# Optimization experiments

Measured on AMD Instinct MI355X. Metric: run time of the kernel, lower is better.

## Reference

```python
import jax, jax.numpy as jnp
import numpy as np

B, C, N, V, W, D = 4, 64, 8, 32, 32, 256  # spa_dim = D


def _ln(x, g, b, eps=1e-5):
    m = jnp.mean(x, -1, keepdims=True)
    v = jnp.mean((x - m) ** 2, -1, keepdims=True)
    return (x - m) * jax.lax.rsqrt(v + eps) * g + b


def _tokens(x):
    # (b, c, n, v, w) -> (b*n, v*w, c)
    b, c, n, v, w = x.shape
    return x.transpose(0, 2, 3, 4, 1).reshape(b * n, v * w, c)


def setup_inputs() -> dict:
    key = jax.random.key(0)
    ks = jax.random.split(key, 8)
    fea_lf = jax.random.normal(ks[0], (B, C, N, V, W), jnp.float32)
    fea_hf = jax.random.normal(ks[1], (B, C, N, V, W), jnp.float32)
    W_in = jax.random.normal(ks[2], (C, D), jnp.float32) / np.sqrt(C)
    W_kv = jax.random.normal(ks[3], (C, 2 * D), jnp.float32) / np.sqrt(C)
    gamma = jnp.ones((D,), jnp.float32)
    beta = jnp.zeros((D,), jnp.float32)
    g2 = jnp.ones((D,), jnp.float32)
    b2 = jnp.zeros((D,), jnp.float32)
    W1 = jax.random.normal(ks[4], (D, 2 * D), jnp.float32) / np.sqrt(D)
    W2 = jax.random.normal(ks[5], (2 * D, D), jnp.float32) / np.sqrt(2 * D)
    W_out = jax.random.normal(ks[6], (D, C), jnp.float32) / np.sqrt(D)
    return {"fea_lf": fea_lf, "fea_hf": fea_hf, "W_in": W_in, "W_kv": W_kv,
            "gamma": gamma, "beta": beta, "g2": g2, "b2": b2,
            "W1": W1, "W2": W2, "W_out": W_out}


def reference(fea_lf, fea_hf, W_in, W_kv, gamma, beta, g2, b2, W1, W2, W_out):
    b, c, n, v, w = fea_lf.shape
    S = v * w
    tok_q = _tokens(fea_lf)   # (bn, S, c)
    tok_kv = _tokens(fea_hf)  # (bn, S, c)
    q = _ln(tok_q @ W_in, gamma, beta)              # (bn, S, D)
    kv = tok_kv @ W_kv
    k, vtok = jnp.split(kv, 2, axis=-1)
    k = _ln(k, gamma, beta)                          # shared LayerNorm (self.norm)
    # NOTE: original has no 1/sqrt(d) scaling on scores.
    score = jnp.einsum('bqd,bkd->bqk', q, k)         # (bn, S, S)
    mask = jnp.tril(jnp.ones((S, S), bool))
    score = jnp.where(mask, score, jnp.float32(-1e15))
    p = jax.nn.softmax(score, axis=-1)
    att = jnp.einsum('bqk,bkd->bqd', p, vtok)        # (bn, S, D)
    h = jax.nn.relu(_ln(att, g2, b2) @ W1) @ W2      # FFN (dropout=0)
    epi = h + vtok
    out = epi @ W_out                                # (bn, S, c)
    return out.reshape(b, n, v, w, c).transpose(0, 4, 1, 2, 3)
```

## Files before the change

kernel.cpp:

```cpp
#include <hip/hip_runtime.h>

typedef short bf16x8 __attribute__((ext_vector_type(8)));
typedef _Float16 f16x8 __attribute__((ext_vector_type(8)));
typedef float f32x4 __attribute__((ext_vector_type(4)));
typedef unsigned short u16;
typedef unsigned short u16x4 __attribute__((ext_vector_type(4)));

#define MFMA(a, b, c) __builtin_amdgcn_mfma_f32_16x16x32_bf16(a, b, c, 0, 0, 0)
#define MFMAH(a, b, c) __builtin_amdgcn_mfma_f32_16x16x32_f16(a, b, c, 0, 0, 0)

__device__ __forceinline__ u16 f2b(float f) {
    union { float f; unsigned u; } x{f};
    unsigned r = (x.u + 0x7FFFu + ((x.u >> 16) & 1u)) >> 16;
    return (u16)r;
}
__device__ __forceinline__ float b2f(u16 h) {
    union { unsigned u; float f; } x{((unsigned)h) << 16};
    return x.f;
}
__device__ __forceinline__ u16 f2h(float f) {
    _Float16 h = (_Float16)f;
    return *reinterpret_cast<u16*>(&h);
}
__device__ __forceinline__ float h2f(u16 h) {
    _Float16 v = *reinterpret_cast<_Float16*>(&h);
    return (float)v;
}
__device__ __forceinline__ float red16_sum(float v) {
#pragma unroll
    for (int m = 1; m < 16; m <<= 1) v += __shfl_xor(v, m, 64);
    return v;
}
__device__ __forceinline__ float red16_max(float v) {
#pragma unroll
    for (int m = 1; m < 16; m <<= 1) v = fmaxf(v, __shfl_xor(v, m, 64));
    return v;
}
__device__ __forceinline__ void gl_lds16(const void* g, void* l) {
    __builtin_amdgcn_global_load_lds(
        (const __attribute__((address_space(1))) unsigned int*)(g),
        (__attribute__((address_space(3))) unsigned int*)(l), 16, 0, 0);
}


__global__ __launch_bounds__(256) void wconv_kernel(
    const float* __restrict__ W1, const float* __restrict__ W2,
    const float* __restrict__ Wo, const float* __restrict__ Win,
    const float* __restrict__ Wkv, u16* __restrict__ w1T,
    u16* __restrict__ w2T, u16* __restrict__ woT, u16* __restrict__ wfrag) {
    int id = blockIdx.x * 256 + threadIdx.x;
    if (id < 131072) {
        int n = id >> 8, k = id & 255;
        w1T[id] = f2b(W1[k * 512 + n]);
    } else if (id < 262144) {
        int j = id - 131072;
        int n = j >> 9, k = j & 511;
        w2T[j] = f2b(W2[k * 256 + n]);
    } else if (id < 278528) {
        int j = id - 262144;
        int n = j >> 8, k = j & 255;
        woT[j] = f2b(Wo[k * 64 + n]);
    } else if (id < 284672) {
        int fid = id - 278528;
        int arr = fid >> 11;
        int e = fid & 2047;
        int ntck = e >> 6, ln = e & 63;
        int lr = ln & 15, lg2 = ln >> 4;
        int nt = ntck >> 1, ck = ntck & 1;
        int d = nt * 16 + lr;
#pragma unroll
        for (int j = 0; j < 8; j++) {
            int c = ck * 32 + lg2 * 8 + j;
            float x;
            if (arr == 0)      x = Win[c * 256 + d];
            else if (arr == 1) x = Wkv[c * 512 + d];
            else               x = Wkv[c * 512 + 256 + d];
            wfrag[arr * 16384 + e * 8 + j] = f2h(x);
        }
    }
}

#define PJ_A 0
#define PJ_WREG 16384
#define PJ_WORK 49152
__global__ __launch_bounds__(512, 1) void proj_kernel(
    const float* __restrict__ lf, const float* __restrict__ hf,
    const u16* __restrict__ wqg, const u16* __restrict__ wkg,
    const u16* __restrict__ wvg, const float* __restrict__ gamma,
    const float* __restrict__ beta, u16* __restrict__ qf_,
    u16* __restrict__ kf_, u16* __restrict__ vT) {
    extern __shared__ char sm[];
    const int tid = threadIdx.x;
    const int wave = tid >> 6, lane = tid & 63, lr = lane & 15, lg = lane >> 4;
    const int st = blockIdx.x, bn = blockIdx.y;
    const int b = bn >> 3, n = bn & 7;
    const int s0 = st * 128;
    const size_t baseF = (size_t)b * 524288 + (size_t)n * 1024 + s0;

    float gam[16], bet[16];
#pragma unroll
    for (int nt = 0; nt < 16; nt++) {
        gam[nt] = gamma[nt * 16 + lr];
        bet[nt] = beta[nt * 16 + lr];
    }

    auto stage32 = [&](const float* srcbase, int chalf) {
#pragma unroll
        for (int call = 0; call < 2; call++) {
            int unit = call * 8 + wave;
            int obase = unit << 10;
            int e = unit * 256 + lane * 4;
            int cl = e >> 7, si = e & 127;
            gl_lds16(srcbase + (size_t)(chalf * 32 + cl) * 8192 + si,
                     sm + PJ_WORK + obase);
        }
    };
    auto stageW = [&](const u16* wsrc) {
#pragma unroll
        for (int call = 0; call < 4; call++) {
            int obase = (call * 8 + wave) << 10;
            gl_lds16((const char*)wsrc + obase + lane * 16, sm + PJ_WREG + obase);
        }
    };
    auto buildA = [&](int slotbase) {
        int g = wave >> 1;
        int s = ((wave & 1) << 6) | lane;
        float x[8];
#pragma unroll
        for (int cc = 0; cc < 8; cc++)
            x[cc] = *(const float*)(sm + PJ_WORK + ((g * 8 + cc) << 9) + (s << 2));
        f16x8 ph;
#pragma unroll
        for (int cc = 0; cc < 8; cc++) ph[cc] = (_Float16)x[cc];
        int slp = (slotbase + g) ^ (s & 7);
        *(f16x8*)(sm + PJ_A + (s << 7) + (slp << 4)) = ph;
    };
    auto loadA = [&](f16x8* aF) {
        int tl = wave * 16 + lr;
#pragma unroll
        for (int ck = 0; ck < 2; ck++) {
            int off = (tl << 7) + ((((ck << 2) | lg) ^ (tl & 7)) << 4);
            aF[ck] = *(const f16x8*)(sm + PJ_A + off);
        }
    };
    auto pass1 = [&](const f16x8* aF, f32x4* acc) {
#pragma unroll
        for (int nt = 0; nt < 16; nt++) acc[nt] = (f32x4){0.f, 0.f, 0.f, 0.f};
#pragma unroll
        for (int nt = 0; nt < 16; nt++) {
#pragma unroll
            for (int ck = 0; ck < 2; ck++) {
                int wo = (((nt << 1) | ck) << 10) + (lane << 4);
                f16x8 bh = *(const f16x8*)(sm + PJ_WREG + wo);
                acc[nt] = MFMAH(aF[ck], bh, acc[nt]);
            }
        }
    };
    auto lnstats = [&](const f32x4* acc, float* mean, float* rs) {
#pragma unroll
        for (int r = 0; r < 4; r++) {
            float s1 = 0.f, s2 = 0.f;
#pragma unroll
            for (int nt = 0; nt < 16; nt++) {
                float xv = acc[nt][r];
                s1 += xv; s2 += xv * xv;
            }
            s1 = red16_sum(s1);
            s2 = red16_sum(s2);
            float mn = s1 * (1.f / 256.f);
            float var = s2 * (1.f / 256.f) - mn * mn;
            mean[r] = mn;
            rs[r] = rsqrtf(var + 1e-5f);
        }
    };
    auto emit = [&](const f32x4* acc, const float* mean, const float* rs,
                    u16* dst) {
        char* bw = sm + PJ_WORK + wave * 4096;
        const int gtok = bn * 1024 + s0 + wave * 16;
#pragma unroll
        for (int hh = 0; hh < 2; hh++) {
#pragma unroll
            for (int ntl = 0; ntl < 8; ntl++) {
                int nt = hh * 8 + ntl;
#pragma unroll
                for (int r = 0; r < 4; r++) {
                    float y = (acc[nt][r] - mean[r]) * rs[r] * gam[nt] + bet[nt];
                    int tl = lg * 4 + r;
                    int dl = ntl * 16 + lr;
                    int sl = dl >> 3;
                    *(u16*)(bw + tl * 256 + ((sl ^ ((tl >> 2) & 3)) << 4) +
                            (dl & 7) * 2) = f2h(y);
                }
            }
#pragma unroll
            for (int p = 0; p < 4; p++) {
                int row = lane >> 2, slq = (lane & 3) + p * 4;
                bf16x8 v8 = *(const bf16x8*)(bw + row * 256 +
                                             ((slq ^ ((row >> 2) & 3)) << 4));
                *(bf16x8*)(dst + (size_t)(gtok + row) * 256 + hh * 128 +
                           slq * 8) = v8;
            }
        }
    };

    f32x4 acc[16];
    float mean[4], rs[4];
    f16x8 aF[2];

    stage32(lf + baseF, 0);  __syncthreads();
    buildA(0);               __syncthreads();
    stage32(lf + baseF, 1);
    stageW(wqg);             __syncthreads();
    buildA(4);               __syncthreads();
    loadA(aF);
    pass1(aF, acc);
    lnstats(acc, mean, rs);  __syncthreads();
    stageW(wkg);
    emit(acc, mean, rs, qf_);
    __syncthreads();
    stage32(hf + baseF, 0);  __syncthreads();
    buildA(0);               __syncthreads();
    stage32(hf + baseF, 1);  __syncthreads();
    buildA(4);               __syncthreads();
    loadA(aF);
    pass1(aF, acc);
    lnstats(acc, mean, rs);  __syncthreads();
    stageW(wvg);
    emit(acc, mean, rs, kf_);
    __syncthreads();
    pass1(aF, acc);
#pragma unroll
    for (int nt = 0; nt < 16; nt++) {
        u16x4 pv;
#pragma unroll
        for (int r = 0; r < 4; r++) pv[r] = f2h(acc[nt][r]);
        *(u16x4*)(vT + ((size_t)(bn * 256) + nt * 16 + lr) * 1024 + s0 +
                  wave * 16 + lg * 4) = pv;
    }
}

__global__ __launch_bounds__(512) void attn_kernel(
    const u16* __restrict__ qf_, const u16* __restrict__ kf_,
    const u16* __restrict__ vT, const float* __restrict__ g2,
    const float* __restrict__ b2, u16* __restrict__ lnatt) {
    extern __shared__ char smem[];
    const int tid = threadIdx.x;
    const int wave = tid >> 6, lane = tid & 63, lr = lane & 15, lg = lane >> 4;
    const int grp = wave >> 2, w4 = wave & 3;
    const int b = blockIdx.x;
    const int bn = b & 31;
    const int strip = 15 - (b >> 5);
    const int qr0 = strip * 64 + w4 * 16;
    const int ni = strip + 1;
    const int ktbase = grp * ni;
    char* myK = smem + grp * 65536;
    char* myV = smem + grp * 65536 + 32768;
    u16* Pw = (u16*)(smem + 131072 + wave * 1280);

    f16x8 qf[8];
    {
        const size_t off = ((size_t)(bn * 1024 + qr0 + lr)) * 256 + lg * 8;
#pragma unroll
        for (int ck = 0; ck < 8; ck++)
            qf[ck] = *(const f16x8*)(qf_ + off + ck * 32);
    }
    f16x8 onesb;
    {
        _Float16 v1 = (lr == 0) ? (_Float16)1.0f : (_Float16)0.0f;
#pragma unroll
        for (int q = 0; q < 8; q++) onesb[q] = v1;
    }

    const int srl = lane >> 5, ss = lane & 31;
    const int vdl = lane >> 2, vg = lane & 3;
    auto stage = [&](int buf, int kt) {
        const int kv0 = kt << 5;
        char* baseK = myK + buf * 16384;
        char* baseV = myV + buf * 16384;
#pragma unroll
        for (int ii = 0; ii < 4; ii++) {
            int u = w4 * 4 + ii;
            int r = u * 2 + srl;
            size_t go = (((size_t)((bn << 10) + kv0 + r)) << 8) +
                        (unsigned)((ss ^ (r & 7)) << 3);
            gl_lds16(kf_ + go, baseK + u * 1024);
            int d = u * 16 + vdl;
            size_t gv = (((size_t)((bn << 8) + d)) << 10) + kv0 +
                        (unsigned)((vg ^ ((d >> 1) & 3)) << 3);
            gl_lds16(vT + gv, baseV + u * 1024);
        }
    };

    f32x4 o[16];
#pragma unroll
    for (int i = 0; i < 16; i++) o[i] = (f32x4){0.f, 0.f, 0.f, 0.f};
    f32x4 ol = (f32x4){0.f, 0.f, 0.f, 0.f};
    float m[4] = {-INFINITY, -INFINITY, -INFINITY, -INFINITY};

    stage(0, ktbase);
    for (int it = 0; it < ni; it++) {
        const int cur = it & 1;
        if (it + 1 < ni) {
            stage(cur ^ 1, ktbase + it + 1);
            asm volatile("s_waitcnt vmcnt(8)" ::: "memory");
        } else {
            asm volatile("s_waitcnt vmcnt(0)" ::: "memory");
        }
        __builtin_amdgcn_s_barrier();
        asm volatile("" ::: "memory");
        const int kt = ktbase + it;
        if ((kt << 5) <= qr0 + 15) {
            const char* kb = myK + cur * 16384;
            f32x4 sc0 = (f32x4){0.f, 0.f, 0.f, 0.f};
            f32x4 sc1 = (f32x4){0.f, 0.f, 0.f, 0.f};
            __builtin_amdgcn_s_setprio(1);
#pragma unroll
            for (int ck = 0; ck < 8; ck++) {
                int sw = ((ck * 4 + lg) ^ (lr & 7)) << 4;
                int a0 = lr * 512 + sw;
                f16x8 k0 = *(const f16x8*)(kb + a0);
                f16x8 k1 = *(const f16x8*)(kb + a0 + 8192);
                sc0 = MFMAH(qf[ck], k0, sc0);
                sc1 = MFMAH(qf[ck], k1, sc1);
            }
            __builtin_amdgcn_s_setprio(0);
            float scl[4];
            const int kvb = kt << 5;
#pragma unroll
            for (int r = 0; r < 4; r++) {
                int qi = qr0 + lg * 4 + r;
                float s0v = (kvb + lr > qi) ? -1e30f : sc0[r];
                float s1v = (kvb + 16 + lr > qi) ? -1e30f : sc1[r];
                float tm = red16_max(fmaxf(s0v, s1v));
                float mn = fmaxf(m[r], tm);
                scl[r] = __expf(m[r] - mn);
                m[r] = mn;
                int row = lg * 4 + r;
                Pw[row * 40 + lr] = f2h(__expf(s0v - mn));
                Pw[row * 40 + 16 + lr] = f2h(__expf(s1v - mn));
            }
#pragma unroll
            for (int f = 0; f < 16; f++) {
                f32x4 t = o[f];
                t[0] *= scl[0]; t[1] *= scl[1]; t[2] *= scl[2]; t[3] *= scl[3];
                o[f] = t;
            }
            ol[0] *= scl[0]; ol[1] *= scl[1]; ol[2] *= scl[2]; ol[3] *= scl[3];
            f16x8 pa = *(const f16x8*)((const char*)Pw + lr * 80 + lg * 16);
            const char* vb = myV + cur * 16384;
            __builtin_amdgcn_s_setprio(1);
#pragma unroll
            for (int db = 0; db < 16; db++) {
                int d = db * 16 + lr;
                f16x8 vf = *(const f16x8*)(vb + d * 64 +
                                           ((lg ^ ((lr >> 1) & 3)) << 4));
                o[db] = MFMAH(pa, vf, o[db]);
            }
            ol = MFMAH(pa, onesb, ol);
            __builtin_amdgcn_s_setprio(0);
        }
    }
    __syncthreads();
    float lsum[4];
#pragma unroll
    for (int r = 0; r < 4; r++) lsum[r] = __shfl(ol[r], lane & 48, 64);

    char* cb = smem + 65536;
    float* mlb = (float*)(smem + 131072);
    if (grp == 1) {
        char* po = cb + w4 * 16384;
#pragma unroll
        for (int f = 0; f < 16; f++)
            *(f32x4*)(po + (f * 16 + lr) * 64 + lg * 16) = o[f];
        if (lr == 0) {
#pragma unroll
            for (int r = 0; r < 4; r++) {
                int row = lg * 4 + r;
                mlb[(w4 * 16 + row) * 2] = m[r];
                mlb[(w4 * 16 + row) * 2 + 1] = lsum[r];
            }
        }
    }
    __syncthreads();
    if (grp == 0) {
        const char* po = cb + w4 * 16384;
        float e0[4], e1[4], linv[4];
#pragma unroll
        for (int r = 0; r < 4; r++) {
            int row = lg * 4 + r;
            float m1 = mlb[(w4 * 16 + row) * 2];
            float l1 = mlb[(w4 * 16 + row) * 2 + 1];
            float ms = fmaxf(m[r], m1);
            e0[r] = __expf(m[r] - ms);
            e1[r] = __expf(m1 - ms);
            linv[r] = 1.f / (lsum[r] * e0[r] + l1 * e1[r]);
        }
#pragma unroll
        for (int f = 0; f < 16; f++) {
            f32x4 o1 = *(const f32x4*)(po + (f * 16 + lr) * 64 + lg * 16);
#pragma unroll
            for (int r = 0; r < 4; r++)
                o[f][r] = (o[f][r] * e0[r] + o1[r] * e1[r]) * linv[r];
        }
        float gv[16], bv[16];
#pragma unroll
        for (int f = 0; f < 16; f++) {
            gv[f] = g2[f * 16 + lr];
            bv[f] = b2[f * 16 + lr];
        }
#pragma unroll
        for (int r = 0; r < 4; r++) {
            float s1 = 0.f, s2 = 0.f;
#pragma unroll
            for (int f = 0; f < 16; f++) {
                float x = o[f][r];
                s1 += x; s2 += x * x;
            }
            s1 = red16_sum(s1);
            s2 = red16_sum(s2);
            float mean = s1 * (1.f / 256.f);
            float var = s2 * (1.f / 256.f) - mean * mean;
            float rsv = rsqrtf(var + 1e-5f);
            size_t row = (size_t)(bn * 1024 + qr0 + lg * 4 + r) * 256;
#pragma unroll
            for (int f = 0; f < 16; f++)
                lnatt[row + f * 16 + lr] =
                    f2b((o[f][r] - mean) * rsv * gv[f] + bv[f]);
        }
    }
}

template <int K, int NB, int MODE>
__global__ __launch_bounds__(512) void gemmB_kernel(
    const u16* __restrict__ A, const u16* __restrict__ BT,
    u16* __restrict__ outb, const u16* __restrict__ vTr,
    float* __restrict__ outf, int ldOut) {
    extern __shared__ char bsm[];
    const int tid = threadIdx.x;
    const int wave = tid >> 6, lane = tid & 63, lr = lane & 15, lg = lane >> 4;
    constexpr int K2 = K * 2;
    constexpr int BN = NB * 16;
    constexpr int TILE = BN * K2;
    const int m0 = blockIdx.x * 128 + wave * 16;
    const int n0 = blockIdx.y * BN;
    {
        const char* bsrc = (const char*)(BT + (size_t)n0 * K);
        constexpr int ITER = TILE / (512 * 16);
#pragma unroll
        for (int it = 0; it < ITER; it++) {
            int o = (it * 512 + tid) * 16;
            int col = o / K2;
            int slot = (o % K2) >> 4;
            int src = col * K2 + ((slot ^ (col & 7)) << 4);
            gl_lds16(bsrc + src, bsm + o);
        }
    }
    __syncthreads();
    f32x4 acc[NB];
#pragma unroll
    for (int nb = 0; nb < NB; nb++) acc[nb] = (f32x4){0.f, 0.f, 0.f, 0.f};
    const u16* ap = A + (size_t)(m0 + lr) * K + lg * 8;
#pragma unroll
    for (int kc = 0; kc < K; kc += 32) {
        bf16x8 a = *(const bf16x8*)(ap + kc);
        int ks = (kc >> 3) + lg;
#pragma unroll
        for (int nb = 0; nb < NB; nb++) {
            int c = nb * 16 + lr;
            bf16x8 bv = *(const bf16x8*)(bsm + c * K2 + ((ks ^ (c & 7)) << 4));
            acc[nb] = MFMA(a, bv, acc[nb]);
        }
    }
    const int g = m0 + lg * 4;
    if (MODE == 0) {
#pragma unroll
        for (int nb = 0; nb < NB; nb++)
#pragma unroll
            for (int r = 0; r < 4; r++)
                outb[(size_t)(g + r) * ldOut + n0 + nb * 16 + lr] =
                    f2b(fmaxf(acc[nb][r], 0.f));
    } else if (MODE == 1) {
        int bn = g >> 10, s = g & 1023;
#pragma unroll
        for (int nb = 0; nb < NB; nb++) {
            int dd = n0 + nb * 16 + lr;
            u16x4 vv = *(const u16x4*)(vTr + ((size_t)bn * 256 + dd) * 1024 + s);
#pragma unroll
            for (int r = 0; r < 4; r++)
                outb[(size_t)(g + r) * 256 + dd] = f2b(acc[nb][r] + h2f(vv[r]));
        }
    } else {
        int bn = g >> 10, s = g & 1023;
        int bb = bn >> 3, nn = bn & 7;
#pragma unroll
        for (int nb = 0; nb < NB; nb++) {
            int cc = n0 + nb * 16 + lr;
            *(f32x4*)(outf + (size_t)bb * 524288 + (size_t)cc * 8192 +
                      (size_t)nn * 1024 + s) = acc[nb];
        }
    }
}

extern "C" void kernel_launch(void* const* d_in, const int* in_sizes, int n_in,
                              void* d_out, int out_size, void* d_ws, size_t ws_size,
                              hipStream_t stream) {
    const float* lf    = (const float*)d_in[0];
    const float* hf    = (const float*)d_in[1];
    const float* Win   = (const float*)d_in[2];
    const float* Wkv   = (const float*)d_in[3];
    const float* gamma = (const float*)d_in[4];
    const float* beta  = (const float*)d_in[5];
    const float* g2    = (const float*)d_in[6];
    const float* b2    = (const float*)d_in[7];
    const float* W1    = (const float*)d_in[8];
    const float* W2    = (const float*)d_in[9];
    const float* Wo    = (const float*)d_in[10];
    float* out = (float*)d_out;

    char* w = (char*)d_ws;
    const size_t MB16 = 16777216;
    u16* qf  = (u16*)(w);
    u16* kf  = (u16*)(w + MB16);
    u16* vT  = (u16*)(w + 2 * MB16);
    u16* hb  = (u16*)(w + 3 * MB16);
    u16* w1T = (u16*)(w + 3 * MB16 + 33554432);
    u16* w2T = w1T + 131072;
    u16* woT = w2T + 131072;
    u16* wfrag = woT + 16384;
    u16* wqg = wfrag;
    u16* wkg = wfrag + 16384;
    u16* wvg = wfrag + 32768;
    u16* lnatt = qf;
    u16* epib  = kf;

    wconv_kernel<<<dim3(1136), dim3(256), 0, stream>>>(W1, W2, Wo, Win, Wkv,
                                                       w1T, w2T, woT, wfrag);
    proj_kernel<<<dim3(8, 32), dim3(512), 81920, stream>>>(
        lf, hf, wqg, wkg, wvg, gamma, beta, qf, kf, vT);
    attn_kernel<<<dim3(512), dim3(512), 141312, stream>>>(qf, kf, vT, g2, b2,
                                                          lnatt);
    gemmB_kernel<256, 8, 0><<<dim3(256, 4), dim3(512), 65536, stream>>>(
        lnatt, w1T, hb, nullptr, nullptr, 512);
    gemmB_kernel<512, 8, 1><<<dim3(256, 2), dim3(512), 131072, stream>>>(
        hb, w2T, epib, vT, nullptr, 256);
    gemmB_kernel<256, 4, 2><<<dim3(256, 1), dim3(512), 32768, stream>>>(
        epib, woT, nullptr, nullptr, out, 64);
}
```

Baseline: 125.9 us.

## Restructure attention into 2-wave blocks with two row tiles per wave, no KV split

The attention kernel drops from 8 waves with a two-group KV split and double-buffered staging to 2 waves per block. Each wave now handles two 16-row query tiles, so every K/V fragment read from shared memory feeds twice as many MFMAs. The cross-group merge of partial softmax results is gone, and LDS use falls from about 138 KB to 37 KB, which allows more resident blocks per CU. In exchange, staging is no longer double-buffered, each block makes a serial pass over all KV tiles with a barrier per step, and register pressure roughly doubles for the accumulators.

```diff
diff --git a/kernel.cpp b/kernel.cpp
--- a/kernel.cpp
+++ b/kernel.cpp
@@ -239,30 +239,27 @@
     }
 }
 
-__global__ __launch_bounds__(512) void attn_kernel(
+__global__ __launch_bounds__(128) void attn_kernel(
     const u16* __restrict__ qf_, const u16* __restrict__ kf_,
     const u16* __restrict__ vT, const float* __restrict__ g2,
     const float* __restrict__ b2, u16* __restrict__ lnatt) {
-    extern __shared__ char smem[];
+    __shared__ char smem[37888];
     const int tid = threadIdx.x;
     const int wave = tid >> 6, lane = tid & 63, lr = lane & 15, lg = lane >> 4;
-    const int grp = wave >> 2, w4 = wave & 3;
     const int b = blockIdx.x;
     const int bn = b & 31;
     const int strip = 15 - (b >> 5);
-    const int qr0 = strip * 64 + w4 * 16;
-    const int ni = strip + 1;
-    const int ktbase = grp * ni;
-    char* myK = smem + grp * 65536;
-    char* myV = smem + grp * 65536 + 32768;
-    u16* Pw = (u16*)(smem + 131072 + wave * 1280);
-
-    f16x8 qf[8];
-    {
-        const size_t off = ((size_t)(bn * 1024 + qr0 + lr)) * 256 + lg * 8;
+    const int qr0 = strip * 64 + wave * 32;
+    const int ni = 2 * strip + 2;
+    u16* Pw = (u16*)(smem + 32768 + wave * 2560);
+
+    f16x8 qf[2][8];
+#pragma unroll
+    for (int rt = 0; rt < 2; rt++) {
+        const size_t off = ((size_t)(bn * 1024 + qr0 + rt * 16 + lr)) * 256 + lg * 8;
 #pragma unroll
         for (int ck = 0; ck < 8; ck++)
-            qf[ck] = *(const f16x8*)(qf_ + off + ck * 32);
+            qf[rt][ck] = *(const f16x8*)(qf_ + off + ck * 32);
     }
     f16x8 onesb;
     {
@@ -271,149 +268,126 @@
         for (int q = 0; q < 8; q++) onesb[q] = v1;
     }
 
-    const int srl = lane >> 5, ss = lane & 31;
-    const int vdl = lane >> 2, vg = lane & 3;
-    auto stage = [&](int buf, int kt) {
+    f32x4 o[2][16];
+#pragma unroll
+    for (int rt = 0; rt < 2; rt++)
+#pragma unroll
+        for (int i = 0; i < 16; i++) o[rt][i] = (f32x4){0.f, 0.f, 0.f, 0.f};
+    f32x4 ol[2] = {(f32x4){0.f, 0.f, 0.f, 0.f}, (f32x4){0.f, 0.f, 0.f, 0.f}};
+    float m[2][4];
+#pragma unroll
+    for (int rt = 0; rt < 2; rt++)
+#pragma unroll
+        for (int r = 0; r < 4; r++) m[rt][r] = -INFINITY;
+
+    for (int kt = 0; kt < ni; kt++) {
         const int kv0 = kt << 5;
-        char* baseK = myK + buf * 16384;
-        char* baseV = myV + buf * 16384;
-#pragma unroll
-        for (int ii = 0; ii < 4; ii++) {
-            int u = w4 * 4 + ii;
-            int r = u * 2 + srl;
+#pragma unroll
+        for (int u = 0; u < 8; u++) {
+            int ob = u * 2048 + tid * 16;
+            int r = ob >> 9;
+            int ss = tid & 31;
             size_t go = (((size_t)((bn << 10) + kv0 + r)) << 8) +
                         (unsigned)((ss ^ (r & 7)) << 3);
-            gl_lds16(kf_ + go, baseK + u * 1024);
-            int d = u * 16 + vdl;
+            gl_lds16(kf_ + go, smem + ob);
+            int d = u * 32 + (tid >> 2);
             size_t gv = (((size_t)((bn << 8) + d)) << 10) + kv0 +
-                        (unsigned)((vg ^ ((d >> 1) & 3)) << 3);
-            gl_lds16(vT + gv, baseV + u * 1024);
-        }
-    };
-
-    f32x4 o[16];
-#pragma unroll
-    for (int i = 0; i < 16; i++) o[i] = (f32x4){0.f, 0.f, 0.f, 0.f};
-    f32x4 ol = (f32x4){0.f, 0.f, 0.f, 0.f};
-    float m[4] = {-INFINITY, -INFINITY, -INFINITY, -INFINITY};
-
-    stage(0, ktbase);
-    for (int it = 0; it < ni; it++) {
-        const int cur = it & 1;
-        if (it + 1 < ni) {
-            stage(cur ^ 1, ktbase + it + 1);
-            asm volatile("s_waitcnt vmcnt(8)" ::: "memory");
-        } else {
-            asm volatile("s_waitcnt vmcnt(0)" ::: "memory");
-        }
-        __builtin_amdgcn_s_barrier();
-        asm volatile("" ::: "memory");
-        const int kt = ktbase + it;
-        if ((kt << 5) <= qr0 + 15) {
-            const char* kb = myK + cur * 16384;
-            f32x4 sc0 = (f32x4){0.f, 0.f, 0.f, 0.f};
-            f32x4 sc1 = (f32x4){0.f, 0.f, 0.f, 0.f};
+                        (unsigned)(((tid & 3) ^ ((d >> 1) & 3)) << 3);
+            gl_lds16(vT + gv, smem + 16384 + u * 2048 + tid * 16);
+        }
+        __syncthreads();
+        if (kv0 <= qr0 + 31) {
+            f32x4 sc00 = (f32x4){0.f, 0.f, 0.f, 0.f};
+            f32x4 sc01 = (f32x4){0.f, 0.f, 0.f, 0.f};
+            f32x4 sc10 = (f32x4){0.f, 0.f, 0.f, 0.f};
+            f32x4 sc11 = (f32x4){0.f, 0.f, 0.f, 0.f};
             __builtin_amdgcn_s_setprio(1);
 #pragma unroll
             for (int ck = 0; ck < 8; ck++) {
                 int sw = ((ck * 4 + lg) ^ (lr & 7)) << 4;
                 int a0 = lr * 512 + sw;
-                f16x8 k0 = *(const f16x8*)(kb + a0);
-                f16x8 k1 = *(const f16x8*)(kb + a0 + 8192);
-                sc0 = MFMAH(qf[ck], k0, sc0);
-                sc1 = MFMAH(qf[ck], k1, sc1);
+                f16x8 k0 = *(const f16x8*)(smem + a0);
+                f16x8 k1 = *(const f16x8*)(smem + a0 + 8192);
+                sc00 = MFMAH(qf[0][ck], k0, sc00);
+                sc01 = MFMAH(qf[0][ck], k1, sc01);
+                sc10 = MFMAH(qf[1][ck], k0, sc10);
+                sc11 = MFMAH(qf[1][ck], k1, sc11);
             }
             __builtin_amdgcn_s_setprio(0);
-            float scl[4];
-            const int kvb = kt << 5;
-#pragma unroll
-            for (int r = 0; r < 4; r++) {
-                int qi = qr0 + lg * 4 + r;
-                float s0v = (kvb + lr > qi) ? -1e30f : sc0[r];
-                float s1v = (kvb + 16 + lr > qi) ? -1e30f : sc1[r];
-                float tm = red16_max(fmaxf(s0v, s1v));
-                float mn = fmaxf(m[r], tm);
-                scl[r] = __expf(m[r] - mn);
-                m[r] = mn;
-                int row = lg * 4 + r;
-                Pw[row * 40 + lr] = f2h(__expf(s0v - mn));
-                Pw[row * 40 + 16 + lr] = f2h(__expf(s1v - mn));
-            }
-#pragma unroll
-            for (int f = 0; f < 16; f++) {
-                f32x4 t = o[f];
-                t[0] *= scl[0]; t[1] *= scl[1]; t[2] *= scl[2]; t[3] *= scl[3];
-                o[f] = t;
-            }
-            ol[0] *= scl[0]; ol[1] *= scl[1]; ol[2] *= scl[2]; ol[3] *= scl[3];
-            f16x8 pa = *(const f16x8*)((const char*)Pw + lr * 80 + lg * 16);
-            const char* vb = myV + cur * 16384;
+            float scl[2][4];
+#pragma unroll
+            for (int rt = 0; rt < 2; rt++) {
+                const f32x4& s0 = rt ? sc10 : sc00;
+                const f32x4& s1 = rt ? sc11 : sc01;
+#pragma unroll
+                for (int r = 0; r < 4; r++) {
+                    int qi = qr0 + rt * 16 + lg * 4 + r;
+                    float s0v = (kv0 + lr > qi) ? -1e30f : s0[r];
+                    float s1v = (kv0 + 16 + lr > qi) ? -1e30f : s1[r];
+                    float tm = red16_max(fmaxf(s0v, s1v));
+                    float mn = fmaxf(m[rt][r], tm);
+                    scl[rt][r] = __expf(m[rt][r] - mn);
+                    m[rt][r] = mn;
+                    int row = rt * 16 + lg * 4 + r;
+                    Pw[row * 40 + lr] = f2h(__expf(s0v - mn));
+                    Pw[row * 40 + 16 + lr] = f2h(__expf(s1v - mn));
+                }
+            }
+#pragma unroll
+            for (int rt = 0; rt < 2; rt++) {
+#pragma unroll
+                for (int f = 0; f < 16; f++) {
+                    f32x4 t = o[rt][f];
+                    t[0] *= scl[rt][0]; t[1] *= scl[rt][1];
+                    t[2] *= scl[rt][2]; t[3] *= scl[rt][3];
+                    o[rt][f] = t;
+                }
+                f32x4 t = ol[rt];
+                t[0] *= scl[rt][0]; t[1] *= scl[rt][1];
+                t[2] *= scl[rt][2]; t[3] *= scl[rt][3];
+                ol[rt] = t;
+            }
+            asm volatile("" ::: "memory");
+            f16x8 pa0 = *(const f16x8*)((const char*)Pw + lr * 80 + lg * 16);
+            f16x8 pa1 = *(const f16x8*)((const char*)Pw + (16 + lr) * 80 + lg * 16);
             __builtin_amdgcn_s_setprio(1);
 #pragma unroll
             for (int db = 0; db < 16; db++) {
                 int d = db * 16 + lr;
-                f16x8 vf = *(const f16x8*)(vb + d * 64 +
+                f16x8 vf = *(const f16x8*)(smem + 16384 + d * 64 +
                                            ((lg ^ ((lr >> 1) & 3)) << 4));
-                o[db] = MFMAH(pa, vf, o[db]);
-            }
-            ol = MFMAH(pa, onesb, ol);
+                o[0][db] = MFMAH(pa0, vf, o[0][db]);
+                o[1][db] = MFMAH(pa1, vf, o[1][db]);
+            }
+            ol[0] = MFMAH(pa0, onesb, ol[0]);
+            ol[1] = MFMAH(pa1, onesb, ol[1]);
             __builtin_amdgcn_s_setprio(0);
         }
-    }
-    __syncthreads();
-    float lsum[4];
-#pragma unroll
-    for (int r = 0; r < 4; r++) lsum[r] = __shfl(ol[r], lane & 48, 64);
-
-    char* cb = smem + 65536;
-    float* mlb = (float*)(smem + 131072);
-    if (grp == 1) {
-        char* po = cb + w4 * 16384;
-#pragma unroll
-        for (int f = 0; f < 16; f++)
-            *(f32x4*)(po + (f * 16 + lr) * 64 + lg * 16) = o[f];
-        if (lr == 0) {
-#pragma unroll
-            for (int r = 0; r < 4; r++) {
-                int row = lg * 4 + r;
-                mlb[(w4 * 16 + row) * 2] = m[r];
-                mlb[(w4 * 16 + row) * 2 + 1] = lsum[r];
-            }
-        }
-    }
-    __syncthreads();
-    if (grp == 0) {
-        const char* po = cb + w4 * 16384;
-        float e0[4], e1[4], linv[4];
-#pragma unroll
-        for (int r = 0; r < 4; r++) {
-            int row = lg * 4 + r;
-            float m1 = mlb[(w4 * 16 + row) * 2];
-            float l1 = mlb[(w4 * 16 + row) * 2 + 1];
-            float ms = fmaxf(m[r], m1);
-            e0[r] = __expf(m[r] - ms);
-            e1[r] = __expf(m1 - ms);
-            linv[r] = 1.f / (lsum[r] * e0[r] + l1 * e1[r]);
-        }
+        __syncthreads();
+    }
+    float gv[16], bv[16];
+#pragma unroll
+    for (int f = 0; f < 16; f++) {
+        gv[f] = g2[f * 16 + lr];
+        bv[f] = b2[f * 16 + lr];
+    }
+#pragma unroll
+    for (int rt = 0; rt < 2; rt++) {
+        float linv[4];
+#pragma unroll
+        for (int r = 0; r < 4; r++)
+            linv[r] = 1.f / __shfl(ol[rt][r], lane & 48, 64);
 #pragma unroll
         for (int f = 0; f < 16; f++) {
-            f32x4 o1 = *(const f32x4*)(po + (f * 16 + lr) * 64 + lg * 16);
-#pragma unroll
-            for (int r = 0; r < 4; r++)
-                o[f][r] = (o[f][r] * e0[r] + o1[r] * e1[r]) * linv[r];
-        }
-        float gv[16], bv[16];
-#pragma unroll
-        for (int f = 0; f < 16; f++) {
-            gv[f] = g2[f * 16 + lr];
-            bv[f] = b2[f * 16 + lr];
+            o[rt][f][0] *= linv[0]; o[rt][f][1] *= linv[1];
+            o[rt][f][2] *= linv[2]; o[rt][f][3] *= linv[3];
         }
 #pragma unroll
         for (int r = 0; r < 4; r++) {
             float s1 = 0.f, s2 = 0.f;
 #pragma unroll
             for (int f = 0; f < 16; f++) {
-                float x = o[f][r];
+                float x = o[rt][f][r];
                 s1 += x; s2 += x * x;
             }
             s1 = red16_sum(s1);
@@ -421,11 +395,11 @@
             float mean = s1 * (1.f / 256.f);
             float var = s2 * (1.f / 256.f) - mean * mean;
             float rsv = rsqrtf(var + 1e-5f);
-            size_t row = (size_t)(bn * 1024 + qr0 + lg * 4 + r) * 256;
+            size_t row = (size_t)(bn * 1024 + qr0 + rt * 16 + lg * 4 + r) * 256;
 #pragma unroll
             for (int f = 0; f < 16; f++)
                 lnatt[row + f * 16 + lr] =
-                    f2b((o[f][r] - mean) * rsv * gv[f] + bv[f]);
+                    f2b((o[rt][f][r] - mean) * rsv * gv[f] + bv[f]);
         }
     }
 }
@@ -537,8 +511,7 @@
                                                        w1T, w2T, woT, wfrag);
     proj_kernel<<<dim3(8, 32), dim3(512), 81920, stream>>>(
         lf, hf, wqg, wkg, wvg, gamma, beta, qf, kf, vT);
-    attn_kernel<<<dim3(512), dim3(512), 141312, stream>>>(qf, kf, vT, g2, b2,
-                                                          lnatt);
+    attn_kernel<<<dim3(512), dim3(128), 0, stream>>>(qf, kf, vT, g2, b2, lnatt);
     gemmB_kernel<256, 8, 0><<<dim3(256, 4), dim3(512), 65536, stream>>>(
         lnatt, w1T, hb, nullptr, nullptr, 512);
     gemmB_kernel<512, 8, 1><<<dim3(256, 2), dim3(512), 131072, stream>>>(
```

New measurement: 186.4 us. +48.1%, slower.
